# Kernel tuning notes

Hardware: AMD Instinct MI355X
Metric: run time of the kernel (lower is better)

The kernel has to match this reference:

```python
import jax, jax.numpy as jnp
import numpy as np

N, E, D, H = 50000, 600000, 128, 128
SLOPE = 0.01  # default negative_slope of F.leaky_relu / nn.LeakyReLU


def leaky(x):
    return jnp.where(x >= 0, x, SLOPE * x)


def gcn_conv(x, src, dst, W, b, n):
    """PyG GCNConv: x' = D^{-1/2}(A+I)D^{-1/2} (x W) + b, symmetric norm with self-loops."""
    h = x @ W  # [n, out]
    ones = jnp.ones(src.shape[0], h.dtype)
    deg = jax.ops.segment_sum(ones, dst, num_segments=n) + 1.0  # +1 for self-loop
    dinv = jax.lax.rsqrt(deg)  # deg >= 1 always
    norm = dinv[src] * dinv[dst]  # per-edge coefficient
    msg = h[src] * norm[:, None]  # gather + scale: [E, out]
    agg = jax.ops.segment_sum(msg, dst, num_segments=n)  # scatter-add
    agg = agg + h * (dinv * dinv)[:, None]  # self-loop term
    return agg + b


def setup_inputs() -> dict:
    key = jax.random.key(0)
    ks = jax.random.split(key, 16)
    kaiming = lambda k, fi, fo: jax.random.normal(k, (fi, fo), jnp.float32) * np.sqrt(2.0 / fi)
    return {
        "x": jax.random.normal(ks[0], (N, D), jnp.float32),
        "edge_index": jax.random.randint(ks[1], (2, E), 0, N, jnp.int64 if jax.config.jax_enable_x64 else jnp.int32),
        "gen_data": jax.random.normal(ks[2], (N, H), jnp.float32),
        "Wc1": kaiming(ks[3], D, H), "bc1": jnp.zeros((H,), jnp.float32),
        "Wc2": kaiming(ks[4], H, H), "bc2": jnp.zeros((H,), jnp.float32),
        "Wm1": kaiming(ks[5], H, H), "bm1": jnp.zeros((H,), jnp.float32),
        "Wm2": kaiming(ks[6], H, H), "bm2": jnp.zeros((H,), jnp.float32),
        "Wp1": kaiming(ks[7], H, H), "bp1": jnp.zeros((H,), jnp.float32),
        "Wp2": kaiming(ks[8], H, H), "bp2": jnp.zeros((H,), jnp.float32),
    }


def reference(x, edge_index, gen_data, Wc1, bc1, Wc2, bc2, Wm1, bm1, Wm2, bm2, Wp1, bp1, Wp2, bp2):
    src, dst = edge_index[0], edge_index[1]
    lambd = 0.5
    # GraphEncoder4Link
    h = leaky(gcn_conv(x, src, dst, Wc1, bc1, N))
    h = leaky(gcn_conv(h, src, dst, Wc2, bc2, N) + h)
    h = leaky((leaky(h @ Wm1 + bm1) @ Wm2 + bm2) + h)
    # lambd interpolation with gen_data
    out = lambd * h + (1.0 - lambd) * gen_data
    # proj MLP
    out = leaky(leaky(out @ Wp1 + bp1) @ Wp2 + bp2)
    return out
```

## Files before the change

### kernel.cpp

```cpp
#include <hip/hip_runtime.h>
#include <cstdint>
#include <cstddef>

#define HH 128
#define SLOPE 0.01f

typedef __attribute__((ext_vector_type(8))) __bf16 bf16x8;
typedef __attribute__((ext_vector_type(8))) unsigned short ushort8v;
typedef __attribute__((ext_vector_type(4))) float f32x4;

__device__ __forceinline__ float lrelu(float x) { return x >= 0.f ? x : SLOPE * x; }
__device__ __forceinline__ unsigned short f2b(float f) {
  union { float f; unsigned u; } v; v.f = f;
  unsigned r = v.u + 0x7fffu + ((v.u >> 16) & 1u);
  return (unsigned short)(r >> 16);
}
__device__ __forceinline__ float b2f(unsigned short u) {
  union { unsigned u; float f; } v; v.u = ((unsigned)u) << 16; return v.f;
}

__device__ __forceinline__ int lofs(int r, int k) {
  return (r << 7) + ((((k >> 3) ^ r) & 15) << 3) + (k & 7);
}

#define WAVE_SYNC() asm volatile("s_waitcnt lgkmcnt(0)" ::: "memory")

__device__ __forceinline__ void gll16(const void* g, void* l) {
  __builtin_amdgcn_global_load_lds((const __attribute__((address_space(1))) void*)g,
                                   (__attribute__((address_space(3))) void*)l, 16, 0, 0);
}


__global__ __launch_bounds__(256) void count_kernel(const int* __restrict__ dst,
                                                    int* __restrict__ cnt,
                                                    int* __restrict__ rank, int nE) {
  int e = blockIdx.x * 256 + threadIdx.x;
  if (e < nE) rank[e] = atomicAdd(&cnt[dst[e]], 1);
}

__global__ __launch_bounds__(1024) void scan1_kernel(int* __restrict__ cnt,
                                                     int* __restrict__ rowptr,
                                                     int* __restrict__ bsum,
                                                     float* __restrict__ dinv, int n) {
  __shared__ int wsum[16];
  const int tid = threadIdx.x;
  const int lane = tid & 63, wid = tid >> 6;
  int i = blockIdx.x * 1024 + tid;
  int v = (i < n) ? cnt[i] : 0;
  int x = v;
#pragma unroll
  for (int off = 1; off < 64; off <<= 1) {
    int y = __shfl_up(x, off, 64);
    if (lane >= off) x += y;
  }
  if (lane == 63) wsum[wid] = x;
  __syncthreads();
  if (tid == 0) {
    int s = 0;
#pragma unroll
    for (int w = 0; w < 16; ++w) { int t = wsum[w]; wsum[w] = s; s += t; }
    bsum[blockIdx.x] = s;
  }
  __syncthreads();
  if (i < n) {
    rowptr[i] = wsum[wid] + x - v;
    dinv[i] = rsqrtf((float)v + 1.0f);
  }
}

__global__ __launch_bounds__(64) void scan2_kernel(int* __restrict__ bsum, int nb,
                                                   int* __restrict__ rowptr, int n, int E) {
  int lane = threadIdx.x;
  int v = (lane < nb) ? bsum[lane] : 0;
  int x = v;
#pragma unroll
  for (int off = 1; off < 64; off <<= 1) {
    int y = __shfl_up(x, off, 64);
    if (lane >= off) x += y;
  }
  if (lane < nb) bsum[lane] = x - v;
  if (lane == 0) rowptr[n] = E;
}

__global__ __launch_bounds__(1024) void scan3_kernel(int* __restrict__ rowptr,
                                                     const int* __restrict__ bsum, int n) {
  int i = blockIdx.x * 1024 + threadIdx.x;
  if (i < n) rowptr[i] += bsum[blockIdx.x];
}

__global__ __launch_bounds__(256) void fill_kernel(const int* __restrict__ src,
                                                   const int* __restrict__ dst,
                                                   const int* __restrict__ rowptr,
                                                   const int* __restrict__ rank,
                                                   const float* __restrict__ dinv,
                                                   int2* __restrict__ csr, int nE) {
  int e = blockIdx.x * 256 + threadIdx.x;
  if (e >= nE) return;
  int d = dst[e], s = src[e];
  int pos = rowptr[d] + rank[e];
  int2 ent;
  ent.x = s;
  ent.y = __float_as_int(dinv[s] * dinv[d]);
  csr[pos] = ent;
}

__global__ __launch_bounds__(256) void pack_kernel(const float* W0, const float* W1,
                                                   const float* W2, const float* W3,
                                                   const float* W4, const float* W5,
                                                   unsigned short* __restrict__ out) {
  const float* Ws[6] = {W0, W1, W2, W3, W4, W5};
  const float* W = Ws[blockIdx.y];
  int f = blockIdx.x * 256 + threadIdx.x;
  int j = f & 7, L = (f >> 3) & 63, c = (f >> 9) & 7, t = f >> 12;
  int k = t * 32 + (L >> 4) * 8 + j;
  int n = c * 16 + (L & 15);
  out[(size_t)blockIdx.y * 16384 + f] = f2b(W[k * HH + n]);
}


__device__ __forceinline__ void mfma_ldsW(const bf16x8 af[4],
                                          const unsigned short* __restrict__ Wl,
                                          int lane, f32x4 acc[8]) {
#pragma unroll
  for (int c = 0; c < 8; ++c) acc[c] = (f32x4){0.f, 0.f, 0.f, 0.f};
#pragma unroll
  for (int t = 0; t < 4; ++t) {
    bf16x8 wf[8];
#pragma unroll
    for (int c = 0; c < 8; ++c) wf[c] = *(const bf16x8*)&Wl[(t * 8 + c) * 512 + lane * 8];
#pragma unroll
    for (int c = 0; c < 8; ++c)
      acc[c] = __builtin_amdgcn_mfma_f32_16x16x32_bf16(af[t], wf[c], acc[c], 0, 0, 0);
  }
}

__device__ __forceinline__ void lds_afrags16(const unsigned short* __restrict__ Tl,
                                             int m, int quad, bf16x8 af[4]) {
#pragma unroll
  for (int t = 0; t < 4; ++t)
    af[t] = *(const bf16x8*)&Tl[lofs(m, t * 32 + quad * 8)];
}


__global__ __launch_bounds__(256, 1) void gemm_conv(const float* __restrict__ A,
                                                    const unsigned short* __restrict__ Wp,
                                                    unsigned short* __restrict__ out, int nrows) {
  __shared__ __align__(16) unsigned short Wl[16384];
  const int tid = threadIdx.x;
  const int lane = tid & 63, wave = tid >> 6;
  const int row0 = blockIdx.x * 64 + wave * 16;
  const int m = lane & 15, quad = lane >> 4;

#pragma unroll
  for (int i = 0; i < 8; ++i)
    gll16((const uint4*)Wp + i * 256 + tid, (uint4*)Wl + i * 256 + wave * 64);

  const int gr = row0 + m;
  const bool rok = gr < nrows;
  const float* Arow = A + (size_t)gr * HH;
  bf16x8 af[4];
#pragma unroll
  for (int t = 0; t < 4; ++t) {
    const int k = t * 32 + quad * 8;
    float4 lo = make_float4(0.f, 0.f, 0.f, 0.f), hi = lo;
    if (rok) {
      lo = *(const float4*)(Arow + k);
      hi = *(const float4*)(Arow + k + 4);
    }
    union { ushort8v u; bf16x8 b; } cv;
    cv.u[0] = f2b(lo.x); cv.u[1] = f2b(lo.y); cv.u[2] = f2b(lo.z); cv.u[3] = f2b(lo.w);
    cv.u[4] = f2b(hi.x); cv.u[5] = f2b(hi.y); cv.u[6] = f2b(hi.z); cv.u[7] = f2b(hi.w);
    af[t] = cv.b;
  }

  __syncthreads();

  f32x4 acc[8];
  mfma_ldsW(af, Wl, lane, acc);

#pragma unroll
  for (int c = 0; c < 8; ++c) {
    int col = c * 16 + m;
#pragma unroll
    for (int g = 0; g < 4; ++g) {
      int row = row0 + quad * 4 + g;
      if (row < nrows) out[(size_t)row * HH + col] = f2b(acc[c][g]);
    }
  }
}


template <int RES, int OUTBF>
__global__ __launch_bounds__(256) void agg_kernel(const unsigned short* __restrict__ h,
                                                  const int* __restrict__ rowptr,
                                                  const int2* __restrict__ csr,
                                                  const float* __restrict__ dinv,
                                                  const float* __restrict__ bias,
                                                  const float* __restrict__ res,
                                                  void* __restrict__ outv, int n) {
  int node = blockIdx.x * 4 + (threadIdx.x >> 6);
  if (node >= n) return;
  const int lane = threadIdx.x & 63;
  const int p = lane >> 5;
  const int c4 = (lane & 31) << 2;
  int j = rowptr[node];
  const int end = rowptr[node + 1];
  float a0 = 0.f, a1 = 0.f, a2 = 0.f, a3 = 0.f;

  for (; j + 8 <= end; j += 8) {
    int2 e[4];
    ushort4 r[4];
#pragma unroll
    for (int q = 0; q < 4; ++q) e[q] = csr[j + 2 * q + p];
#pragma unroll
    for (int q = 0; q < 4; ++q) r[q] = *(const ushort4*)(h + (size_t)e[q].x * HH + c4);
#pragma unroll
    for (int q = 0; q < 4; ++q) {
      float nv = __int_as_float(e[q].y);
      a0 = fmaf(b2f(r[q].x), nv, a0); a1 = fmaf(b2f(r[q].y), nv, a1);
      a2 = fmaf(b2f(r[q].z), nv, a2); a3 = fmaf(b2f(r[q].w), nv, a3);
    }
  }
  for (; j + 2 <= end; j += 2) {
    int2 e = csr[j + p];
    ushort4 r = *(const ushort4*)(h + (size_t)e.x * HH + c4);
    float nv = __int_as_float(e.y);
    a0 = fmaf(b2f(r.x), nv, a0); a1 = fmaf(b2f(r.y), nv, a1);
    a2 = fmaf(b2f(r.z), nv, a2); a3 = fmaf(b2f(r.w), nv, a3);
  }
  if (j < end && p == 0) {
    int2 e = csr[j];
    ushort4 r = *(const ushort4*)(h + (size_t)e.x * HH + c4);
    float nv = __int_as_float(e.y);
    a0 = fmaf(b2f(r.x), nv, a0); a1 = fmaf(b2f(r.y), nv, a1);
    a2 = fmaf(b2f(r.z), nv, a2); a3 = fmaf(b2f(r.w), nv, a3);
  }

  a0 += __shfl_xor(a0, 32);
  a1 += __shfl_xor(a1, 32);
  a2 += __shfl_xor(a2, 32);
  a3 += __shfl_xor(a3, 32);

  if (p == 0) {
    float di = dinv[node], d2 = di * di;
    ushort4 hs = *(const ushort4*)(h + (size_t)node * HH + c4);
    float4 b = *(const float4*)(bias + c4);
    float o0 = a0 + b2f(hs.x) * d2 + b.x;
    float o1 = a1 + b2f(hs.y) * d2 + b.y;
    float o2 = a2 + b2f(hs.z) * d2 + b.z;
    float o3 = a3 + b2f(hs.w) * d2 + b.w;
    if (RES) {
      float4 r = *(const float4*)(res + (size_t)node * HH + c4);
      o0 += r.x; o1 += r.y; o2 += r.z; o3 += r.w;
    }
    o0 = lrelu(o0); o1 = lrelu(o1); o2 = lrelu(o2); o3 = lrelu(o3);
    if (OUTBF) {
      ushort4 o;
      o.x = f2b(o0); o.y = f2b(o1); o.z = f2b(o2); o.w = f2b(o3);
      *(ushort4*)((unsigned short*)outv + (size_t)node * HH + c4) = o;
    } else {
      *(float4*)((float*)outv + (size_t)node * HH + c4) = make_float4(o0, o1, o2, o3);
    }
  }
}


__global__ __launch_bounds__(256, 1) void fusedMLP(const unsigned short* __restrict__ f2bf,
                                                   const unsigned short* __restrict__ Wm1p,
                                                   const unsigned short* __restrict__ Wm2p,
                                                   const unsigned short* __restrict__ Wp1p,
                                                   const unsigned short* __restrict__ Wp2p,
                                                   const float* __restrict__ bm1,
                                                   const float* __restrict__ bm2,
                                                   const float* __restrict__ bp1,
                                                   const float* __restrict__ bp2,
                                                   const float* __restrict__ gen,
                                                   float* __restrict__ out, int n) {
  __shared__ __align__(16) unsigned short Wl[16384];
  __shared__ __align__(16) unsigned short Ta[4][16 * HH];
  __shared__ __align__(16) unsigned short Tb[4][16 * HH];
  __shared__ __align__(16) float Bi[4][4 * HH];
  const int tid = threadIdx.x;
  const int lane = tid & 63, wave = tid >> 6;
  const int row0 = blockIdx.x * 64 + wave * 16;
  const int m = lane & 15, quad = lane >> 4;
  unsigned short* TA = Ta[wave];
  unsigned short* TB = Tb[wave];
  float* BI = Bi[wave];

#pragma unroll
  for (int i = 0; i < 8; ++i)
    gll16((const uint4*)Wm1p + i * 256 + tid, (uint4*)Wl + i * 256 + wave * 64);

#pragma unroll
  for (int i = 0; i < 4; ++i) {
    int idx = i * 64 + lane;
    int r = idx >> 4, k = (idx & 15) << 3;
    int gr = row0 + r;
    ushort8v v = {0, 0, 0, 0, 0, 0, 0, 0};
    if (gr < n) v = *(const ushort8v*)(f2bf + (size_t)gr * HH + k);
    *(ushort8v*)&TA[lofs(r, k)] = v;
  }

  ushort4 genb[8];
#pragma unroll
  for (int i = 0; i < 8; ++i) {
    int idx = i * 64 + lane;
    int r = idx >> 5, c4 = (idx & 31) << 2;
    int gr = row0 + r;
    float4 v = make_float4(0.f, 0.f, 0.f, 0.f);
    if (gr < n) v = *(const float4*)(gen + (size_t)gr * HH + c4);
    genb[i].x = f2b(v.x); genb[i].y = f2b(v.y); genb[i].z = f2b(v.z); genb[i].w = f2b(v.w);
  }

  {
    const float* b01 = (lane < 32) ? bm1 : bm2;
    const float* b23 = (lane < 32) ? bp1 : bp2;
    int col = (lane & 31) << 2;
    float4 v0 = *(const float4*)(b01 + col);
    float4 v1 = *(const float4*)(b23 + col);
    *(float4*)&BI[lane * 4] = v0;
    *(float4*)&BI[256 + lane * 4] = v1;
  }

  __syncthreads();

  bf16x8 af[4];
  f32x4 acc[8];
  float bv[8];

#pragma unroll
  for (int cc = 0; cc < 8; ++cc) bv[cc] = BI[cc * 16 + m];
  lds_afrags16(TA, m, quad, af);
  mfma_ldsW(af, Wl, lane, acc);
#pragma unroll
  for (int cc = 0; cc < 8; ++cc) {
    int col = cc * 16 + m;
#pragma unroll
    for (int g = 0; g < 4; ++g)
      TB[lofs(quad * 4 + g, col)] = f2b(lrelu(acc[cc][g] + bv[cc]));
  }
  __syncthreads();

#pragma unroll
  for (int i = 0; i < 8; ++i)
    gll16((const uint4*)Wm2p + i * 256 + tid, (uint4*)Wl + i * 256 + wave * 64);
#pragma unroll
  for (int cc = 0; cc < 8; ++cc) bv[cc] = BI[128 + cc * 16 + m];
  lds_afrags16(TB, m, quad, af);
  WAVE_SYNC();
#pragma unroll
  for (int i = 0; i < 8; ++i) {
    int idx = i * 64 + lane;
    int r = idx >> 5, c4 = (idx & 31) << 2;
    *(ushort4*)&TB[lofs(r, c4)] = genb[i];
  }
  __syncthreads();

  mfma_ldsW(af, Wl, lane, acc);
#pragma unroll
  for (int cc = 0; cc < 8; ++cc) {
    int col = cc * 16 + m;
#pragma unroll
    for (int g = 0; g < 4; ++g) {
      int lr = quad * 4 + g;
      float f2v = b2f(TA[lofs(lr, col)]);
      float v = lrelu(acc[cc][g] + bv[cc] + f2v);
      float gv = b2f(TB[lofs(lr, col)]);
      TA[lofs(lr, col)] = f2b(0.5f * (v + gv));
    }
  }
  __syncthreads();

#pragma unroll
  for (int i = 0; i < 8; ++i)
    gll16((const uint4*)Wp1p + i * 256 + tid, (uint4*)Wl + i * 256 + wave * 64);
#pragma unroll
  for (int cc = 0; cc < 8; ++cc) bv[cc] = BI[256 + cc * 16 + m];
  lds_afrags16(TA, m, quad, af);
  __syncthreads();

  mfma_ldsW(af, Wl, lane, acc);
#pragma unroll
  for (int cc = 0; cc < 8; ++cc) {
    int col = cc * 16 + m;
#pragma unroll
    for (int g = 0; g < 4; ++g)
      TB[lofs(quad * 4 + g, col)] = f2b(lrelu(acc[cc][g] + bv[cc]));
  }
  __syncthreads();

#pragma unroll
  for (int i = 0; i < 8; ++i)
    gll16((const uint4*)Wp2p + i * 256 + tid, (uint4*)Wl + i * 256 + wave * 64);
#pragma unroll
  for (int cc = 0; cc < 8; ++cc) bv[cc] = BI[384 + cc * 16 + m];
  lds_afrags16(TB, m, quad, af);
  __syncthreads();

  mfma_ldsW(af, Wl, lane, acc);
#pragma unroll
  for (int cc = 0; cc < 8; ++cc) {
    int col = cc * 16 + m;
#pragma unroll
    for (int g = 0; g < 4; ++g) {
      int row = row0 + quad * 4 + g;
      if (row < n) out[(size_t)row * HH + col] = lrelu(acc[cc][g] + bv[cc]);
    }
  }
}


extern "C" void kernel_launch(void* const* d_in, const int* in_sizes, int n_in,
                              void* d_out, int out_size, void* d_ws, size_t ws_size,
                              hipStream_t stream) {
  const float* x   = (const float*)d_in[0];
  const int* ei    = (const int*)d_in[1];
  const float* gen = (const float*)d_in[2];
  const float* Wc1 = (const float*)d_in[3];
  const float* bc1 = (const float*)d_in[4];
  const float* Wc2 = (const float*)d_in[5];
  const float* bc2 = (const float*)d_in[6];
  const float* Wm1 = (const float*)d_in[7];
  const float* bm1 = (const float*)d_in[8];
  const float* Wm2 = (const float*)d_in[9];
  const float* bm2 = (const float*)d_in[10];
  const float* Wp1 = (const float*)d_in[11];
  const float* bp1 = (const float*)d_in[12];
  const float* Wp2 = (const float*)d_in[13];
  const float* bp2 = (const float*)d_in[14];

  const int N = in_sizes[0] / HH;
  const int E = in_sizes[1] / 2;
  const int* src = ei;
  const int* dst = ei + E;

  char* ws = (char*)d_ws;
  size_t off = 0;
  auto alloc = [&](size_t bytes) { void* p = ws + off; off += (bytes + 255) & ~(size_t)255; return p; };
  float* dinv            = (float*)alloc((size_t)N * 4);
  int*   rowptr          = (int*)  alloc((size_t)(N + 1) * 4);
  int*   cnt             = (int*)  alloc((size_t)N * 4);
  int*   bsum            = (int*)  alloc((size_t)64 * 4);
  int*   rank            = (int*)  alloc((size_t)E * 4);
  int2*  csr             = (int2*) alloc((size_t)E * 8);
  unsigned short* h_bf   = (unsigned short*)alloc((size_t)N * HH * 2);
  unsigned short* t2_bf  = (unsigned short*)alloc((size_t)N * HH * 2);
  unsigned short* f2_bf  = (unsigned short*)alloc((size_t)N * HH * 2);
  float* f1_f32          = (float*)alloc((size_t)N * HH * 4);
  unsigned short* packed = (unsigned short*)alloc((size_t)6 * 16384 * 2);
  float* fOut = (float*)d_out;

  const int cblocks = (N + 63) / 64;
  const int eblocks = (E + 255) / 256;
  const int ablocks = (N + 3) / 4;
  const int sblocks = (N + 1023) / 1024;

  pack_kernel<<<dim3(64, 6), 256, 0, stream>>>(Wc1, Wc2, Wm1, Wm2, Wp1, Wp2, packed);

  hipMemsetAsync(cnt, 0, (size_t)N * 4, stream);
  count_kernel<<<eblocks, 256, 0, stream>>>(dst, cnt, rank, E);
  scan1_kernel<<<sblocks, 1024, 0, stream>>>(cnt, rowptr, bsum, dinv, N);
  scan2_kernel<<<1, 64, 0, stream>>>(bsum, sblocks, rowptr, N, E);
  scan3_kernel<<<sblocks, 1024, 0, stream>>>(rowptr, bsum, N);
  fill_kernel<<<eblocks, 256, 0, stream>>>(src, dst, rowptr, rank, dinv, csr, E);

  gemm_conv<<<cblocks, 256, 0, stream>>>(x, packed + 0 * 16384, h_bf, N);
  agg_kernel<0, 0><<<ablocks, 256, 0, stream>>>(h_bf, rowptr, csr, dinv, bc1, nullptr, f1_f32, N);
  gemm_conv<<<cblocks, 256, 0, stream>>>(f1_f32, packed + 1 * 16384, t2_bf, N);
  agg_kernel<1, 1><<<ablocks, 256, 0, stream>>>(t2_bf, rowptr, csr, dinv, bc2, f1_f32, f2_bf, N);
  fusedMLP<<<cblocks, 256, 0, stream>>>(f2_bf,
                                        packed + 2 * 16384, packed + 3 * 16384,
                                        packed + 4 * 16384, packed + 5 * 16384,
                                        bm1, bm2, bp1, bp2, gen, fOut, N);
}
```

Baseline: 277.5 us.

## Pad CSR rows to multiples of eight and drop aggregation tail loops

The degree scan now rounds each node's edge count up to a multiple of 8. The CSR buffer is enlarged and zero-filled, so padded slots hold source 0 with weight 0. This lets the aggregation kernel run only its 8-wide unrolled loop, with no divergent remainder loops. The self-loop, bias and residual loads are also hoisted ahead of the edge loop to overlap their latency. In exchange it adds a multi-megabyte memset and extra wasted gathers on padded slots, which all read row 0.

Result: no change. 278.0 us (+0.2%).

```diff
diff --git a/kernel.cpp b/kernel.cpp
--- a/kernel.cpp
+++ b/kernel.cpp
@@ -47,7 +47,8 @@
   const int lane = tid & 63, wid = tid >> 6;
   int i = blockIdx.x * 1024 + tid;
   int v = (i < n) ? cnt[i] : 0;
-  int x = v;
+  int vp = (v + 7) & ~7;
+  int x = vp;
 #pragma unroll
   for (int off = 1; off < 64; off <<= 1) {
     int y = __shfl_up(x, off, 64);
@@ -63,13 +64,13 @@
   }
   __syncthreads();
   if (i < n) {
-    rowptr[i] = wsum[wid] + x - v;
+    rowptr[i] = wsum[wid] + x - vp;
     dinv[i] = rsqrtf((float)v + 1.0f);
   }
 }
 
 __global__ __launch_bounds__(64) void scan2_kernel(int* __restrict__ bsum, int nb,
-                                                   int* __restrict__ rowptr, int n, int E) {
+                                                   int* __restrict__ rowptr, int n) {
   int lane = threadIdx.x;
   int v = (lane < nb) ? bsum[lane] : 0;
   int x = v;
@@ -78,8 +79,9 @@
     int y = __shfl_up(x, off, 64);
     if (lane >= off) x += y;
   }
+  int tot = __shfl(x, nb - 1);
   if (lane < nb) bsum[lane] = x - v;
-  if (lane == 0) rowptr[n] = E;
+  if (lane == 0) rowptr[n] = tot;
 }
 
 __global__ __launch_bounds__(1024) void scan3_kernel(int* __restrict__ rowptr,
@@ -205,9 +207,15 @@
   const int c4 = (lane & 31) << 2;
   int j = rowptr[node];
   const int end = rowptr[node + 1];
+
+  const float di = dinv[node];
+  const ushort4 hs = *(const ushort4*)(h + (size_t)node * HH + c4);
+  const float4 b = *(const float4*)(bias + c4);
+  float4 rr = make_float4(0.f, 0.f, 0.f, 0.f);
+  if (RES) rr = *(const float4*)(res + (size_t)node * HH + c4);
+
   float a0 = 0.f, a1 = 0.f, a2 = 0.f, a3 = 0.f;
-
-  for (; j + 8 <= end; j += 8) {
+  for (; j < end; j += 8) {
     int2 e[4];
     ushort4 r[4];
 #pragma unroll
@@ -221,20 +229,6 @@
       a2 = fmaf(b2f(r[q].z), nv, a2); a3 = fmaf(b2f(r[q].w), nv, a3);
     }
   }
-  for (; j + 2 <= end; j += 2) {
-    int2 e = csr[j + p];
-    ushort4 r = *(const ushort4*)(h + (size_t)e.x * HH + c4);
-    float nv = __int_as_float(e.y);
-    a0 = fmaf(b2f(r.x), nv, a0); a1 = fmaf(b2f(r.y), nv, a1);
-    a2 = fmaf(b2f(r.z), nv, a2); a3 = fmaf(b2f(r.w), nv, a3);
-  }
-  if (j < end && p == 0) {
-    int2 e = csr[j];
-    ushort4 r = *(const ushort4*)(h + (size_t)e.x * HH + c4);
-    float nv = __int_as_float(e.y);
-    a0 = fmaf(b2f(r.x), nv, a0); a1 = fmaf(b2f(r.y), nv, a1);
-    a2 = fmaf(b2f(r.z), nv, a2); a3 = fmaf(b2f(r.w), nv, a3);
-  }
 
   a0 += __shfl_xor(a0, 32);
   a1 += __shfl_xor(a1, 32);
@@ -242,17 +236,11 @@
   a3 += __shfl_xor(a3, 32);
 
   if (p == 0) {
-    float di = dinv[node], d2 = di * di;
-    ushort4 hs = *(const ushort4*)(h + (size_t)node * HH + c4);
-    float4 b = *(const float4*)(bias + c4);
-    float o0 = a0 + b2f(hs.x) * d2 + b.x;
-    float o1 = a1 + b2f(hs.y) * d2 + b.y;
-    float o2 = a2 + b2f(hs.z) * d2 + b.z;
-    float o3 = a3 + b2f(hs.w) * d2 + b.w;
-    if (RES) {
-      float4 r = *(const float4*)(res + (size_t)node * HH + c4);
-      o0 += r.x; o1 += r.y; o2 += r.z; o3 += r.w;
-    }
+    const float d2 = di * di;
+    float o0 = a0 + b2f(hs.x) * d2 + b.x + rr.x;
+    float o1 = a1 + b2f(hs.y) * d2 + b.y + rr.y;
+    float o2 = a2 + b2f(hs.z) * d2 + b.z + rr.z;
+    float o3 = a3 + b2f(hs.w) * d2 + b.w + rr.w;
     o0 = lrelu(o0); o1 = lrelu(o1); o2 = lrelu(o2); o3 = lrelu(o3);
     if (OUTBF) {
       ushort4 o;
@@ -435,6 +423,8 @@
   const int* src = ei;
   const int* dst = ei + E;
 
+  const size_t Epad = (size_t)E + 8 * (size_t)N;
+
   char* ws = (char*)d_ws;
   size_t off = 0;
   auto alloc = [&](size_t bytes) { void* p = ws + off; off += (bytes + 255) & ~(size_t)255; return p; };
@@ -443,7 +433,7 @@
   int*   cnt             = (int*)  alloc((size_t)N * 4);
   int*   bsum            = (int*)  alloc((size_t)64 * 4);
   int*   rank            = (int*)  alloc((size_t)E * 4);
-  int2*  csr             = (int2*) alloc((size_t)E * 8);
+  int2*  csr             = (int2*) alloc(Epad * 8);
   unsigned short* h_bf   = (unsigned short*)alloc((size_t)N * HH * 2);
   unsigned short* t2_bf  = (unsigned short*)alloc((size_t)N * HH * 2);
   unsigned short* f2_bf  = (unsigned short*)alloc((size_t)N * HH * 2);
@@ -459,9 +449,10 @@
   pack_kernel<<<dim3(64, 6), 256, 0, stream>>>(Wc1, Wc2, Wm1, Wm2, Wp1, Wp2, packed);
 
   hipMemsetAsync(cnt, 0, (size_t)N * 4, stream);
+  hipMemsetAsync(csr, 0, Epad * 8, stream);
   count_kernel<<<eblocks, 256, 0, stream>>>(dst, cnt, rank, E);
   scan1_kernel<<<sblocks, 1024, 0, stream>>>(cnt, rowptr, bsum, dinv, N);
-  scan2_kernel<<<1, 64, 0, stream>>>(bsum, sblocks, rowptr, N, E);
+  scan2_kernel<<<1, 64, 0, stream>>>(bsum, sblocks, rowptr, N);
   scan3_kernel<<<sblocks, 1024, 0, stream>>>(rowptr, bsum, N);
   fill_kernel<<<eblocks, 256, 0, stream>>>(src, dst, rowptr, rank, dinv, csr, E);
 
```
